# Performance work log

Measured on AMD Instinct MI355X. Metric: run time of the kernel, lower is better.

Reference implementation:

```python
import jax, jax.numpy as jnp
import numpy as np

BITS = 8
QMAX = float(2 ** (BITS - 1) - 1)  # 127 for 8-bit symmetric


def bits_quant(x):
    """8-bit symmetric per-tensor fake quantization (models the opaque bits_quant op)."""
    max_abs = jnp.max(jnp.abs(x))
    scale = jnp.where(max_abs > 0, max_abs / QMAX, 1.0).astype(x.dtype)
    q = jnp.clip(jnp.round(x / scale), -QMAX, QMAX) * scale
    return q


def quant_linear(x, w, b):
    # Q(Q(x @ w) + Q(b)) then Q of the result, per QuantLinearLayer.call
    y = bits_quant(jnp.matmul(x, w)) + bits_quant(b)
    return bits_quant(y)


def setup_inputs() -> dict:
    d = 4096
    key = jax.random.key(0)
    ks = jax.random.split(key, 12)
    s = 0.02
    return {
        "inputs": jax.random.normal(ks[0], (1, d), dtype=jnp.float32),
        "c": jax.random.normal(ks[1], (1, d), dtype=jnp.float32) * s,
        "h": jax.random.normal(ks[2], (1, d), dtype=jnp.float32) * s,
        "Wf_w": jax.random.normal(ks[3], (2 * d, d), dtype=jnp.float32) * s,
        "Wf_b": jax.random.normal(ks[4], (d,), dtype=jnp.float32) * s,
        "Wi_w": jax.random.normal(ks[5], (2 * d, d), dtype=jnp.float32) * s,
        "Wi_b": jax.random.normal(ks[6], (d,), dtype=jnp.float32) * s,
        "Wc_w": jax.random.normal(ks[7], (2 * d, d), dtype=jnp.float32) * s,
        "Wc_b": jax.random.normal(ks[8], (d,), dtype=jnp.float32) * s,
        "Wo_w": jax.random.normal(ks[9], (2 * d, d), dtype=jnp.float32) * s,
        "Wo_b": jax.random.normal(ks[10], (d,), dtype=jnp.float32) * s,
    }


def reference(inputs, c, h, Wf_w, Wf_b, Wi_w, Wi_b, Wc_w, Wc_b, Wo_w, Wo_b):
    # concat = Q([h, x])  -> [1, 2d]
    concat = bits_quant(jnp.concatenate([h, inputs], axis=1))
    z = bits_quant(jnp.tanh(quant_linear(concat, Wc_w, Wc_b)))
    zf = bits_quant(jax.nn.sigmoid(quant_linear(concat, Wf_w, Wf_b)))
    zi = bits_quant(jax.nn.sigmoid(quant_linear(concat, Wi_w, Wi_b)))
    zo = bits_quant(jax.nn.sigmoid(quant_linear(concat, Wo_w, Wo_b)))
    memory = bits_quant(z * zi)
    c_new = bits_quant(bits_quant(c * zf) + memory)
    h_new = bits_quant(zo * bits_quant(jnp.tanh(c_new)))
    return h_new
```

## Files before the change

### kernel.cpp

```cpp
#include <hip/hip_runtime.h>
#include <math.h>

#define QMAXF 127.0f

struct Ptrs4 { const float* p[4]; };

__device__ __forceinline__ float qscale(float m) {
    return (m > 0.0f) ? (m / QMAXF) : 1.0f;
}

__device__ __forceinline__ float quant1(float x, float s) {
    float r = rintf(x / s);
    r = fminf(fmaxf(r, -QMAXF), QMAXF);
    return r * s;
}

__device__ __forceinline__ float block_max_red(float v, float* sred) {
    #pragma unroll
    for (int off = 32; off > 0; off >>= 1)
        v = fmaxf(v, __shfl_down(v, off, 64));
    int wave = threadIdx.x >> 6;
    int lane = threadIdx.x & 63;
    __syncthreads();
    if (lane == 0) sred[wave] = v;
    __syncthreads();
    if (threadIdx.x == 0) {
        int nw = blockDim.x >> 6;
        float m = sred[0];
        for (int i = 1; i < nw; ++i) m = fmaxf(m, sred[i]);
        sred[16] = m;
    }
    __syncthreads();
    return sred[16];
}

__device__ __forceinline__ void quant_vec4(float* a, float* sred) {
    float pm = 0.0f;
    #pragma unroll
    for (int i = 0; i < 4; ++i) pm = fmaxf(pm, fabsf(a[i]));
    float s = qscale(block_max_red(pm, sred));
    #pragma unroll
    for (int i = 0; i < 4; ++i) a[i] = quant1(a[i], s);
}

__global__ __launch_bounds__(1024) void k_prep(
    const float* __restrict__ x, const float* __restrict__ h,
    Ptrs4 biases, float* __restrict__ concat_q, float* __restrict__ qb,
    unsigned* __restrict__ gmax)
{
    __shared__ float sred[17];
    int tid = threadIdx.x;
    if (blockIdx.x == 0) {
        if (tid < 4) gmax[tid] = 0u;
        float vals[8];
        float pm = 0.0f;
        #pragma unroll
        for (int i = 0; i < 8; ++i) {
            int idx = i * 1024 + tid;
            float v = (i < 4) ? h[idx] : x[idx - 4096];
            vals[i] = v;
            pm = fmaxf(pm, fabsf(v));
        }
        float s = qscale(block_max_red(pm, sred));
        #pragma unroll
        for (int i = 0; i < 8; ++i) concat_q[i * 1024 + tid] = quant1(vals[i], s);
    } else {
        int g = blockIdx.x - 1;
        const float* __restrict__ b = biases.p[g];
        float vals[4];
        float pm = 0.0f;
        #pragma unroll
        for (int i = 0; i < 4; ++i) {
            float v = b[i * 1024 + tid];
            vals[i] = v;
            pm = fmaxf(pm, fabsf(v));
        }
        float s = qscale(block_max_red(pm, sred));
        #pragma unroll
        for (int i = 0; i < 4; ++i) qb[g * 4096 + i * 1024 + tid] = quant1(vals[i], s);
    }
}

__global__ __launch_bounds__(256, 4) void k_gemv(
    Ptrs4 wts, const float* __restrict__ xq, float* __restrict__ partials)
{
    int ct = blockIdx.x;
    int kc = blockIdx.y;
    int g  = blockIdx.z;
    const float* __restrict__ W = wts.p[g];
    int col0 = ct * 512 + threadIdx.x * 2;
    int k0 = kc * 256;
    const float* __restrict__ wrow = W + (size_t)k0 * 4096 + col0;
    const float* __restrict__ xp = xq + k0;

    float ax = 0.f, ay = 0.f;

    for (int kb = 0; kb < 256; kb += 16) {
        float2 b[16];
        #pragma unroll
        for (int i = 0; i < 16; ++i)
            b[i] = *(const float2*)(wrow + (size_t)(kb + i) * 4096);
        asm volatile("" ::: "memory");
        #pragma unroll
        for (int i = 0; i < 16; ++i) {
            float xv = xp[kb + i];
            ax = fmaf(xv, b[i].x, ax);
            ay = fmaf(xv, b[i].y, ay);
        }
    }

    float2 r; r.x = ax; r.y = ay;
    *(float2*)(partials + (size_t)(g * 32 + kc) * 4096 + col0) = r;
}

__global__ __launch_bounds__(256) void k_reduce(
    const float* __restrict__ partials, float* __restrict__ y,
    unsigned* __restrict__ gmax)
{
    int g  = blockIdx.x >> 4;
    int cb = blockIdx.x & 15;
    int col = cb * 256 + threadIdx.x;
    float s = 0.0f;
    #pragma unroll 8
    for (int kc = 0; kc < 32; ++kc)
        s += partials[(size_t)(g * 32 + kc) * 4096 + col];
    y[g * 4096 + col] = s;

    float m = fabsf(s);
    #pragma unroll
    for (int off = 32; off > 0; off >>= 1)
        m = fmaxf(m, __shfl_down(m, off, 64));
    __shared__ float sm[4];
    int wave = threadIdx.x >> 6, lane = threadIdx.x & 63;
    if (lane == 0) sm[wave] = m;
    __syncthreads();
    if (threadIdx.x == 0) {
        float mm = fmaxf(fmaxf(sm[0], sm[1]), fmaxf(sm[2], sm[3]));
        atomicMax(gmax + g, __float_as_uint(mm));
    }
}

__global__ __launch_bounds__(1024) void k_epilogue(
    const float* __restrict__ y, const float* __restrict__ qb,
    const unsigned* __restrict__ gmax, const float* __restrict__ c,
    float* __restrict__ out)
{
    __shared__ float sred[17];
    int tid = threadIdx.x;
    float v[4][4];

    #pragma unroll
    for (int g = 0; g < 4; ++g) {
        float s = qscale(__uint_as_float(gmax[g]));
        #pragma unroll
        for (int i = 0; i < 4; ++i) {
            int col = i * 1024 + tid;
            v[g][i] = quant1(y[g * 4096 + col], s) + qb[g * 4096 + col];
        }
    }

    for (int g = 0; g < 4; ++g) {
        float pm = 0.0f;
        #pragma unroll
        for (int i = 0; i < 4; ++i) pm = fmaxf(pm, fabsf(v[g][i]));
        float s = qscale(block_max_red(pm, sred));
        #pragma unroll
        for (int i = 0; i < 4; ++i) {
            float q = quant1(v[g][i], s);
            v[g][i] = (g == 2) ? tanhf(q) : (1.0f / (1.0f + expf(-q)));
        }
    }

    for (int g = 0; g < 4; ++g) {
        float pm = 0.0f;
        #pragma unroll
        for (int i = 0; i < 4; ++i) pm = fmaxf(pm, fabsf(v[g][i]));
        float s = qscale(block_max_red(pm, sred));
        #pragma unroll
        for (int i = 0; i < 4; ++i) v[g][i] = quant1(v[g][i], s);
    }

    float mem[4];
    #pragma unroll
    for (int i = 0; i < 4; ++i) mem[i] = v[2][i] * v[1][i];
    quant_vec4(mem, sred);

    float cf[4];
    #pragma unroll
    for (int i = 0; i < 4; ++i) cf[i] = c[i * 1024 + tid] * v[0][i];
    quant_vec4(cf, sred);

    float cn[4];
    #pragma unroll
    for (int i = 0; i < 4; ++i) cn[i] = cf[i] + mem[i];
    quant_vec4(cn, sred);

    float tc[4];
    #pragma unroll
    for (int i = 0; i < 4; ++i) tc[i] = tanhf(cn[i]);
    quant_vec4(tc, sred);

    float hn[4];
    #pragma unroll
    for (int i = 0; i < 4; ++i) hn[i] = v[3][i] * tc[i];
    quant_vec4(hn, sred);
    #pragma unroll
    for (int i = 0; i < 4; ++i) out[i * 1024 + tid] = hn[i];
}

extern "C" void kernel_launch(void* const* d_in, const int* in_sizes, int n_in,
                              void* d_out, int out_size, void* d_ws, size_t ws_size,
                              hipStream_t stream) {
    const float* x = (const float*)d_in[0];
    const float* c = (const float*)d_in[1];
    const float* h = (const float*)d_in[2];
    Ptrs4 wts, bs;
    wts.p[0] = (const float*)d_in[3];  bs.p[0] = (const float*)d_in[4];
    wts.p[1] = (const float*)d_in[5];  bs.p[1] = (const float*)d_in[6];
    wts.p[2] = (const float*)d_in[7];  bs.p[2] = (const float*)d_in[8];
    wts.p[3] = (const float*)d_in[9];  bs.p[3] = (const float*)d_in[10];

    float* ws = (float*)d_ws;
    float* partials = ws;
    float* concat_q = ws + 524288;
    float* qb       = ws + 532480;
    float* yv       = ws + 548864;
    unsigned* gmax  = (unsigned*)(ws + 565248);

    hipLaunchKernelGGL(k_prep,     dim3(5),        dim3(1024), 0, stream,
                       x, h, bs, concat_q, qb, gmax);
    hipLaunchKernelGGL(k_gemv,     dim3(8, 32, 4), dim3(256),  0, stream,
                       wts, concat_q, partials);
    hipLaunchKernelGGL(k_reduce,   dim3(64),       dim3(256),  0, stream,
                       partials, yv, gmax);
    hipLaunchKernelGGL(k_epilogue, dim3(1),        dim3(1024), 0, stream,
                       yv, qb, gmax, c, (float*)d_out);
}
```

Measured before the change: 482.3 us.

## Double-buffer GEMV weight tiles through LDS with direct global-to-LDS loads

The GEMV kernel now stages 8-row weight tiles into a double-buffered shared-memory area using global_load_lds, prefetching the next tile while the current one is consumed. This replaces per-thread register batches of 16 float2 loads. The aim is to overlap memory fetches with FMAs and use wider 16-byte transfers. In exchange it adds a block barrier every 8 rows, uses 32 KB of LDS per block, and keeps fewer bytes in flight per stage than the old register batching.

```diff
diff --git a/kernel.cpp b/kernel.cpp
--- a/kernel.cpp
+++ b/kernel.cpp
@@ -84,31 +84,53 @@
 __global__ __launch_bounds__(256, 4) void k_gemv(
     Ptrs4 wts, const float* __restrict__ xq, float* __restrict__ partials)
 {
+    __shared__ float buf[2][8 * 512];
+
     int ct = blockIdx.x;
     int kc = blockIdx.y;
     int g  = blockIdx.z;
     const float* __restrict__ W = wts.p[g];
-    int col0 = ct * 512 + threadIdx.x * 2;
+    int tid  = threadIdx.x;
+    int wave = tid >> 6;
+    int lane = tid & 63;
     int k0 = kc * 256;
-    const float* __restrict__ wrow = W + (size_t)k0 * 4096 + col0;
+    const float* __restrict__ wbase = W + (size_t)k0 * 4096 + ct * 512;
     const float* __restrict__ xp = xq + k0;
 
+    auto stage = [&](const float* wsrc, float* lbuf) {
+        #pragma unroll
+        for (int j = 0; j < 4; ++j) {
+            int t = wave * 4 + j;
+            int row = t >> 1, half = t & 1;
+            const float* src = wsrc + (size_t)row * 4096 + half * 256 + lane * 4;
+            float* dst = lbuf + row * 512 + half * 256;
+            __builtin_amdgcn_global_load_lds(
+                (const __attribute__((address_space(1))) void*)src,
+                (__attribute__((address_space(3))) void*)dst, 16, 0, 0);
+        }
+    };
+
     float ax = 0.f, ay = 0.f;
 
-    for (int kb = 0; kb < 256; kb += 16) {
-        float2 b[16];
-        #pragma unroll
-        for (int i = 0; i < 16; ++i)
-            b[i] = *(const float2*)(wrow + (size_t)(kb + i) * 4096);
-        asm volatile("" ::: "memory");
-        #pragma unroll
-        for (int i = 0; i < 16; ++i) {
-            float xv = xp[kb + i];
-            ax = fmaf(xv, b[i].x, ax);
-            ay = fmaf(xv, b[i].y, ay);
-        }
-    }
-
+    stage(wbase, buf[0]);
+    __syncthreads();
+    int cur = 0;
+
+    for (int kb = 0; kb < 256; kb += 8) {
+        if (kb + 8 < 256)
+            stage(wbase + (size_t)(kb + 8) * 4096, buf[cur ^ 1]);
+        #pragma unroll
+        for (int r = 0; r < 8; ++r) {
+            float xv = xp[kb + r];
+            float2 wv = *(const float2*)&buf[cur][r * 512 + tid * 2];
+            ax = fmaf(xv, wv.x, ax);
+            ay = fmaf(xv, wv.y, ay);
+        }
+        __syncthreads();
+        cur ^= 1;
+    }
+
+    int col0 = ct * 512 + tid * 2;
     float2 r; r.x = ax; r.y = ay;
     *(float2*)(partials + (size_t)(g * 32 + kc) * 4096 + col0) = r;
 }
```

Result: faster. 461.8 us (-4.3%).
